# Performance work log

Measured on AMD Instinct MI355X. Metric: run time of the kernel, lower is better.

The kernel has to match this reference:

```python
import jax, jax.numpy as jnp
import numpy as np

B_NW, N, DIM, NH, DH, HID, NW, WH = 2048, 64, 512, 16, 32, 384, 64, 8
EPS = 1e-12  # F.normalize eps

def _rel_coords_log(wh, ww):
    # torch.cartesian_prod order: i (rows) outer, j (cols) inner
    ii, jj = np.meshgrid(np.arange(wh), np.arange(ww), indexing='ij')
    coords = np.stack([ii.ravel(), jj.ravel()], axis=-1).astype(np.float32)  # [N,2]
    rel = coords[:, None, :] - coords[None, :, :]                            # [N,N,2]
    return (np.sign(rel) * np.log1p(np.abs(rel))).astype(np.float32)

def setup_inputs() -> dict:
    key = jax.random.key(0)
    ks = jax.random.split(key, 9)
    s = 0.02
    inner = NH * DH
    return {
        'x': jax.random.normal(ks[0], (B_NW, N, DIM), jnp.float32),
        'mask': jax.random.normal(ks[1], (NW, N, N), jnp.float32),
        'w_qkv': jax.random.normal(ks[2], (DIM, 3 * inner), jnp.float32) * s,
        'tau': jnp.ones((1, NH, 1, 1), jnp.float32),
        'mlp_w1': jax.random.normal(ks[3], (2, HID), jnp.float32) * s,
        'mlp_b1': jnp.zeros((HID,), jnp.float32),
        'mlp_w2': jax.random.normal(ks[4], (HID, NH), jnp.float32) * s,
        'mlp_b2': jnp.zeros((NH,), jnp.float32),
        'w_out': jax.random.normal(ks[5], (inner, DIM), jnp.float32) * s,
        'b_out': jnp.zeros((DIM,), jnp.float32),
        'rel_log': jnp.asarray(_rel_coords_log(WH, WH)),
    }

def reference(x, mask, w_qkv, tau, mlp_w1, mlp_b1, mlp_w2, mlp_b2, w_out, b_out, rel_log):
    b, n, _ = x.shape
    qkv = x @ w_qkv                                   # [b, n, 3*nh*dh]
    qkv = qkv.reshape(b, n, 3, NH, DH)
    q, k, v = (jnp.transpose(qkv[:, :, i], (0, 2, 1, 3)) for i in range(3))  # [b, nh, n, dh]
    # cosine attention: L2-normalize q and k along head dim
    q = q / jnp.maximum(jnp.linalg.norm(q, axis=-1, keepdims=True), EPS)
    k = k / jnp.maximum(jnp.linalg.norm(k, axis=-1, keepdims=True), EPS)
    sim = jnp.einsum('bhid,bhjd->bhij', q, k) * tau   # learned temperature
    # relative position bias via meta MLP: [N,N,2] -> [N,N,nh]
    bias = jax.nn.relu(rel_log @ mlp_w1 + mlp_b1) @ mlp_w2 + mlp_b2
    sim = sim + jnp.transpose(bias, (2, 0, 1))[None]  # [1, nh, N, N]
    nw = mask.shape[0]
    sim = sim.reshape(b // nw, nw, NH, n, n) + mask[None, :, None]
    sim = sim.reshape(b, NH, n, n)
    attn = jax.nn.softmax(sim, axis=-1)
    out = jnp.einsum('bhij,bhjd->bhid', attn, v)
    out = jnp.transpose(out, (0, 2, 1, 3)).reshape(b, n, NH * DH)
    return out @ w_out + b_out
```

## Files before the change

### kernel.cpp

```cpp
#include <hip/hip_runtime.h>
#include <hip/hip_bf16.h>


typedef __bf16 bf16;
typedef __bf16 v4bf __attribute__((ext_vector_type(4)));
typedef __bf16 v8bf __attribute__((ext_vector_type(8)));
typedef float  v4f  __attribute__((ext_vector_type(4)));

__global__ void convert_x_kernel(const float* __restrict__ x, bf16* __restrict__ xbf) {
    const int stride = gridDim.x * 256;
    for (size_t idx = blockIdx.x * 256 + threadIdx.x; idx < 8388608; idx += stride) {
        const float4* xv = (const float4*)x;
        float4 v0 = xv[idx * 2];
        float4 v1 = xv[idx * 2 + 1];
        v8bf o = { (bf16)v0.x, (bf16)v0.y, (bf16)v0.z, (bf16)v0.w,
                   (bf16)v1.x, (bf16)v1.y, (bf16)v1.z, (bf16)v1.w };
        *(v8bf*)(xbf + idx * 8) = o;
    }
}

__global__ void convert_w_kernel(const float* __restrict__ wqkv, const float* __restrict__ wout,
                                 bf16* __restrict__ Wt, bf16* __restrict__ WoT) {
    int idx = blockIdx.x * 256 + threadIdx.x;
    Wt[idx] = (bf16)wqkv[(idx & 511) * 1536 + (idx >> 9)];
    if (idx < 262144) WoT[idx] = (bf16)wout[(idx & 511) * 512 + (idx >> 9)];
}

__global__ void bias_kernel(const float* __restrict__ rel_log, const float* __restrict__ w1,
                            const float* __restrict__ b1, const float* __restrict__ w2,
                            const float* __restrict__ b2, float* __restrict__ bias) {
    int p = blockIdx.x * 256 + threadIdx.x;
    float ra = rel_log[p * 2 + 0];
    float rb = rel_log[p * 2 + 1];
    float acc[16];
    #pragma unroll
    for (int t = 0; t < 16; ++t) acc[t] = 0.f;
    for (int kk = 0; kk < 384; ++kk) {
        float hv = fmaxf(ra * w1[kk] + rb * w1[384 + kk] + b1[kk], 0.f);
        #pragma unroll
        for (int t = 0; t < 16; ++t) acc[t] += hv * w2[kk * 16 + t];
    }
    #pragma unroll
    for (int t = 0; t < 16; ++t) bias[t * 4096 + p] = acc[t] + b2[t];
}

__global__ void comb_kernel(const float* __restrict__ bias, const float* __restrict__ mask,
                            float* __restrict__ comb) {
    int idx = blockIdx.x * 256 + threadIdx.x;
    int t = idx & 4095, wh = idx >> 12;
    int w = wh >> 4, h = wh & 15;
    int ij = t >> 8, rem = t & 255;
    int q16 = rem >> 2, r = t & 3;
    int lq = q16 >> 4, lm = q16 & 15;
    int i = ij >> 2, j = ij & 3;
    int p = (i * 16 + lq * 4 + r) * 64 + j * 16 + lm;
    comb[idx] = bias[h * 4096 + p] + mask[w * 4096 + p];
}

__global__ __launch_bounds__(256) void qkv_gemm_kernel(
    const bf16* __restrict__ xbf,
    const bf16* __restrict__ Wt,
    const float* __restrict__ tau,
    bf16* __restrict__ q_ws, bf16* __restrict__ k_ws, bf16* __restrict__ v_ws)
{
    __shared__ alignas(16) bf16 Alds[2][128 * 32];
    __shared__ alignas(16) bf16 Blds[2][128 * 32];
    const int bid = blockIdx.x, nwg = gridDim.x;
    const int wid = (bid & 7) * (nwg >> 3) + (bid >> 3);
    const int nb = wid % 12, mb = wid / 12;

    const int t = threadIdx.x;
    const int wv = t >> 6, lane = t & 63, lq = lane >> 4, lm = lane & 15;
    const int wr = wv >> 1, wc = wv & 1;

    const char* aBase = (const char*)xbf + (size_t)mb * 128 * 1024;
    const char* bBase = (const char*)Wt + (size_t)nb * 128 * 1024;

    auto stage = [&](int buf, int kt) {
        #pragma unroll
        for (int p = 0; p < 2; ++p) {
            int idx = (p * 4 + wv) * 1024 + lane * 16;
            int row = idx >> 6, kb = idx & 63;
            __builtin_amdgcn_global_load_lds(
                (const __attribute__((address_space(1))) void*)(aBase + (size_t)row * 1024 + kt * 64 + kb),
                (__attribute__((address_space(3))) void*)((char*)Alds + buf * 8192 + (p * 4 + wv) * 1024),
                16, 0, 0);
            __builtin_amdgcn_global_load_lds(
                (const __attribute__((address_space(1))) void*)(bBase + (size_t)row * 1024 + kt * 64 + kb),
                (__attribute__((address_space(3))) void*)((char*)Blds + buf * 8192 + (p * 4 + wv) * 1024),
                16, 0, 0);
        }
    };

    v4f acc[4][4];
    #pragma unroll
    for (int i = 0; i < 4; ++i)
        #pragma unroll
        for (int j = 0; j < 4; ++j) acc[i][j] = v4f{0.f, 0.f, 0.f, 0.f};

    stage(0, 0);
    __syncthreads();
    int cur = 0;
    for (int kt = 0; kt < 16; ++kt) {
        if (kt < 15) stage(cur ^ 1, kt + 1);
        v8bf af[4], bfj[4];
        #pragma unroll
        for (int i = 0; i < 4; ++i)
            af[i] = *(const v8bf*)(&Alds[cur][0] + (wr * 64 + i * 16 + lm) * 32 + lq * 8);
        #pragma unroll
        for (int j = 0; j < 4; ++j)
            bfj[j] = *(const v8bf*)(&Blds[cur][0] + (wc * 64 + j * 16 + lm) * 32 + lq * 8);
        #pragma unroll
        for (int i = 0; i < 4; ++i)
            #pragma unroll
            for (int j = 0; j < 4; ++j)
                acc[i][j] = __builtin_amdgcn_mfma_f32_16x16x32_bf16(af[i], bfj[j], acc[i][j], 0, 0, 0);
        __syncthreads();
        cur ^= 1;
    }

    const int bw = mb * 2 + wr;
    if (nb < 8) {
        bf16* dst = (nb < 4) ? q_ws : k_ws;
        const int hbase = (nb & 3) * 4 + wc * 2;
        #pragma unroll
        for (int tpair = 0; tpair < 2; ++tpair) {
            const int h = hbase + tpair;
            const float sc_top = (nb < 4) ? tau[h] : 1.0f;
            #pragma unroll
            for (int i = 0; i < 4; ++i)
                #pragma unroll
                for (int r = 0; r < 4; ++r) {
                    float a0 = acc[i][2 * tpair][r], a1 = acc[i][2 * tpair + 1][r];
                    float ss = a0 * a0 + a1 * a1;
                    #pragma unroll
                    for (int m = 1; m < 16; m <<= 1) ss += __shfl_xor(ss, m);
                    float sc = sc_top / fmaxf(sqrtf(ss), 1e-12f);
                    int n = i * 16 + lq * 4 + r;
                    size_t base = ((size_t)(bw * 16 + h) * 64 + n) * 32;
                    dst[base + lm]      = (bf16)(a0 * sc);
                    dst[base + 16 + lm] = (bf16)(a1 * sc);
                }
        }
    } else {
        #pragma unroll
        for (int j = 0; j < 4; ++j) {
            const int h = (nb - 8) * 4 + wc * 2 + (j >> 1);
            const int dh = (j & 1) * 16 + lm;
            #pragma unroll
            for (int i = 0; i < 4; ++i) {
                v4bf pv = { (bf16)acc[i][j][0], (bf16)acc[i][j][1],
                            (bf16)acc[i][j][2], (bf16)acc[i][j][3] };
                *(v4bf*)(v_ws + ((size_t)(bw * 16 + h) * 32 + dh) * 64 + i * 16 + lq * 4) = pv;
            }
        }
    }
}

__global__ __launch_bounds__(256) void attn_kernel(
    const bf16* __restrict__ q_ws,
    const bf16* __restrict__ k_ws,
    const bf16* __restrict__ v_ws,
    const float* __restrict__ comb,
    int wofs,
    bf16* __restrict__ attn_out)
{
    __shared__ alignas(16) bf16 P_all[4][64 * 72];
    const int blk = blockIdx.x;
    const int b = blk >> 2, g = blk & 3;
    const int tid = threadIdx.x;
    const int wv = tid >> 6, lane = tid & 63, lq = lane >> 4, lm = lane & 15;
    const int h = g * 4 + wv;
    const v4f z4 = {0.f, 0.f, 0.f, 0.f};

    bf16* P = P_all[wv];
    const size_t qk_base = (size_t)(b * 16 + h) * 64 * 32;
    const float* comb_hw = comb + ((size_t)(((wofs + b) & 63) * 16 + h)) * 4096
                                + (lq * 16 + lm) * 4;

    v8bf qf[4], kf[4];
    #pragma unroll
    for (int i = 0; i < 4; ++i)
        qf[i] = *(const v8bf*)(q_ws + qk_base + (i * 16 + lm) * 32 + lq * 8);
    #pragma unroll
    for (int j = 0; j < 4; ++j)
        kf[j] = *(const v8bf*)(k_ws + qk_base + (j * 16 + lm) * 32 + lq * 8);

    v4f s[4][4];
    #pragma unroll
    for (int i = 0; i < 4; ++i)
        #pragma unroll
        for (int j = 0; j < 4; ++j)
            s[i][j] = __builtin_amdgcn_mfma_f32_16x16x32_bf16(qf[i], kf[j], z4, 0, 0, 0);

    #pragma unroll
    for (int i = 0; i < 4; ++i)
        #pragma unroll
        for (int j = 0; j < 4; ++j) {
            float4 cv = *(const float4*)(comb_hw + (i * 4 + j) * 256);
            s[i][j][0] += cv.x; s[i][j][1] += cv.y;
            s[i][j][2] += cv.z; s[i][j][3] += cv.w;
        }

    float rcpl[4][4];
    #pragma unroll
    for (int i = 0; i < 4; ++i) {
        float mx[4], sm[4];
        #pragma unroll
        for (int r = 0; r < 4; ++r) {
            mx[r] = fmaxf(fmaxf(s[i][0][r], s[i][1][r]), fmaxf(s[i][2][r], s[i][3][r]));
            #pragma unroll
            for (int m = 1; m < 16; m <<= 1) mx[r] = fmaxf(mx[r], __shfl_xor(mx[r], m));
            sm[r] = 0.f;
        }
        #pragma unroll
        for (int j = 0; j < 4; ++j)
            #pragma unroll
            for (int r = 0; r < 4; ++r) {
                s[i][j][r] = __expf(s[i][j][r] - mx[r]);
                sm[r] += s[i][j][r];
            }
        #pragma unroll
        for (int r = 0; r < 4; ++r) {
            #pragma unroll
            for (int m = 1; m < 16; m <<= 1) sm[r] += __shfl_xor(sm[r], m);
            rcpl[i][r] = 1.0f / sm[r];
        }
    }

    #pragma unroll
    for (int i = 0; i < 4; ++i)
        #pragma unroll
        for (int j = 0; j < 4; ++j)
            #pragma unroll
            for (int r = 0; r < 4; ++r)
                P[(i * 16 + lq * 4 + r) * 72 + j * 16 + lm] = (bf16)s[i][j][r];

    const size_t v_base = (size_t)(b * 16 + h) * 32 * 64;
    v4f o[4][2];
    #pragma unroll
    for (int i = 0; i < 4; ++i)
        #pragma unroll
        for (int nt = 0; nt < 2; ++nt) o[i][nt] = z4;
    #pragma unroll
    for (int kk = 0; kk < 2; ++kk) {
        v8bf vf[2], pf[4];
        #pragma unroll
        for (int nt = 0; nt < 2; ++nt)
            vf[nt] = *(const v8bf*)(v_ws + v_base + (nt * 16 + lm) * 64 + kk * 32 + lq * 8);
        #pragma unroll
        for (int i = 0; i < 4; ++i)
            pf[i] = *(const v8bf*)(P + (i * 16 + lm) * 72 + kk * 32 + lq * 8);
        #pragma unroll
        for (int i = 0; i < 4; ++i)
            #pragma unroll
            for (int nt = 0; nt < 2; ++nt)
                o[i][nt] = __builtin_amdgcn_mfma_f32_16x16x32_bf16(pf[i], vf[nt], o[i][nt], 0, 0, 0);
    }
    #pragma unroll
    for (int i = 0; i < 4; ++i)
        #pragma unroll
        for (int nt = 0; nt < 2; ++nt)
            #pragma unroll
            for (int r = 0; r < 4; ++r)
                attn_out[(size_t)(b * 64 + i * 16 + lq * 4 + r) * 512 + h * 32 + nt * 16 + lm] =
                    (bf16)(o[i][nt][r] * rcpl[i][r]);
}

__global__ __launch_bounds__(256) void proj_gemm_kernel(
    const bf16* __restrict__ A,
    const bf16* __restrict__ Bt,
    const float* __restrict__ b_out,
    float* __restrict__ out)
{
    __shared__ alignas(16) bf16 Alds[2][128 * 32];
    __shared__ alignas(16) bf16 Blds[2][128 * 32];
    const int bid = blockIdx.x;
    const int wid = (bid & 7) * 512 + (bid >> 3);
    const int mb = wid >> 2, nb = wid & 3;
    const int tid = threadIdx.x;
    const int wv = tid >> 6, lane = tid & 63, lq = lane >> 4, lm = lane & 15;
    const int wr = wv >> 1, wc = wv & 1;

    const char* aBase = (const char*)A + (size_t)mb * 128 * 1024;
    const char* bBase = (const char*)Bt + (size_t)nb * 128 * 1024;

    auto stage = [&](int buf, int kt) {
        #pragma unroll
        for (int p = 0; p < 2; ++p) {
            int idx = (p * 4 + wv) * 1024 + lane * 16;
            int row = idx >> 6, kb = idx & 63;
            __builtin_amdgcn_global_load_lds(
                (const __attribute__((address_space(1))) void*)(aBase + (size_t)row * 1024 + kt * 64 + kb),
                (__attribute__((address_space(3))) void*)((char*)Alds + buf * 8192 + (p * 4 + wv) * 1024),
                16, 0, 0);
            __builtin_amdgcn_global_load_lds(
                (const __attribute__((address_space(1))) void*)(bBase + (size_t)row * 1024 + kt * 64 + kb),
                (__attribute__((address_space(3))) void*)((char*)Blds + buf * 8192 + (p * 4 + wv) * 1024),
                16, 0, 0);
        }
    };

    v4f acc[4][4];
    #pragma unroll
    for (int i = 0; i < 4; ++i)
        #pragma unroll
        for (int j = 0; j < 4; ++j) acc[i][j] = v4f{0.f, 0.f, 0.f, 0.f};

    stage(0, 0);
    __syncthreads();
    int cur = 0;
    for (int kt = 0; kt < 16; ++kt) {
        if (kt < 15) stage(cur ^ 1, kt + 1);
        v8bf af[4], bfj[4];
        #pragma unroll
        for (int i = 0; i < 4; ++i)
            af[i] = *(const v8bf*)(&Alds[cur][0] + (wr * 64 + i * 16 + lm) * 32 + lq * 8);
        #pragma unroll
        for (int j = 0; j < 4; ++j)
            bfj[j] = *(const v8bf*)(&Blds[cur][0] + (wc * 64 + j * 16 + lm) * 32 + lq * 8);
        #pragma unroll
        for (int i = 0; i < 4; ++i)
            #pragma unroll
            for (int j = 0; j < 4; ++j)
                acc[i][j] = __builtin_amdgcn_mfma_f32_16x16x32_bf16(af[i], bfj[j], acc[i][j], 0, 0, 0);
        __syncthreads();
        cur ^= 1;
    }

    #pragma unroll
    for (int j = 0; j < 4; ++j) {
        int col = nb * 128 + wc * 64 + j * 16 + lm;
        float bo = b_out[col];
        #pragma unroll
        for (int i = 0; i < 4; ++i)
            #pragma unroll
            for (int r = 0; r < 4; ++r)
                out[(size_t)(mb * 128 + wr * 64 + i * 16 + lq * 4 + r) * 512 + col] = acc[i][j][r] + bo;
    }
}

extern "C" void kernel_launch(void* const* d_in, const int* in_sizes, int n_in,
                              void* d_out, int out_size, void* d_ws, size_t ws_size,
                              hipStream_t stream) {
    (void)in_sizes; (void)n_in; (void)out_size;
    const float* x       = (const float*)d_in[0];
    const float* mask    = (const float*)d_in[1];
    const float* w_qkv   = (const float*)d_in[2];
    const float* tau     = (const float*)d_in[3];
    const float* mlp_w1  = (const float*)d_in[4];
    const float* mlp_b1  = (const float*)d_in[5];
    const float* mlp_w2  = (const float*)d_in[6];
    const float* mlp_b2  = (const float*)d_in[7];
    const float* w_out   = (const float*)d_in[8];
    const float* b_out   = (const float*)d_in[9];
    const float* rel_log = (const float*)d_in[10];
    float* out = (float*)d_out;

    char* ws = (char*)d_ws;
    bf16*  Wt     = (bf16*)(ws);
    bf16*  WoT    = (bf16*)(ws + 1572864);
    float* bias   = (float*)(ws + 2097152);
    float* comb   = (float*)(ws + 2359296);
    bf16*  shared = (bf16*)(ws + 19136512);
    char*  qkv_base = ws + 153354240;

    size_t avail = (ws_size > 153354240ULL) ? ws_size - 153354240ULL : 0;
    int W = 1024;
    while (W > 128 && (size_t)W * 196608ULL > avail) W >>= 1;
    const size_t qkbuf = (size_t)W * 65536;
    bf16* qb = (bf16*)qkv_base;
    bf16* kb = (bf16*)(qkv_base + qkbuf);
    bf16* vb = (bf16*)(qkv_base + 2 * qkbuf);

    convert_w_kernel<<<3072, 256, 0, stream>>>(w_qkv, w_out, Wt, WoT);
    bias_kernel<<<16, 256, 0, stream>>>(rel_log, mlp_w1, mlp_b1, mlp_w2, mlp_b2, bias);
    comb_kernel<<<16384, 256, 0, stream>>>(bias, mask, comb);
    convert_x_kernel<<<2048, 256, 0, stream>>>(x, shared);

    const int nchunk = 2048 / W;
    for (int c = 0; c < nchunk; ++c) {
        bf16* slice = shared + (size_t)c * W * 64 * 512;
        qkv_gemm_kernel<<<6 * W, 256, 0, stream>>>(slice, Wt, tau, qb, kb, vb);
        attn_kernel<<<4 * W, 256, 0, stream>>>(qb, kb, vb, comb, c * W, slice);
    }
    proj_gemm_kernel<<<4096, 256, 0, stream>>>(shared, WoT, b_out, out);
}
```

Measured before the change: 849.7 us.

## Move q/k normalization into attention and compute transposed scores for cheaper softmax

Removes the per-row L2 normalization (16-lane shuffle reductions) from the QKV GEMM epilogue and instead normalizes q and k fragments in the attention kernel, where each row needs only two cross-lane shuffles. The score matrix is now computed as K·Qᵀ so each lane holds a query row's values along the register axis, which makes the softmax max and sum reductions mostly in-register with two shuffles. The combined bias/mask layout is permuted to match. P is written to shared memory with vectorized 4-wide stores, already normalized, so the final output scaling goes away. Normalization now happens after bf16 rounding of raw q/k, which slightly changes precision, and the bias permutation must exactly match the new fragment layout.

```diff
diff --git a/kernel.cpp b/kernel.cpp
--- a/kernel.cpp
+++ b/kernel.cpp
@@ -49,18 +49,17 @@
     int idx = blockIdx.x * 256 + threadIdx.x;
     int t = idx & 4095, wh = idx >> 12;
     int w = wh >> 4, h = wh & 15;
-    int ij = t >> 8, rem = t & 255;
+    int ji = t >> 8, rem = t & 255;
+    int j = ji >> 2, i = ji & 3;
     int q16 = rem >> 2, r = t & 3;
     int lq = q16 >> 4, lm = q16 & 15;
-    int i = ij >> 2, j = ij & 3;
-    int p = (i * 16 + lq * 4 + r) * 64 + j * 16 + lm;
+    int p = (i * 16 + lm) * 64 + j * 16 + lq * 4 + r;
     comb[idx] = bias[h * 4096 + p] + mask[w * 4096 + p];
 }
 
 __global__ __launch_bounds__(256) void qkv_gemm_kernel(
     const bf16* __restrict__ xbf,
     const bf16* __restrict__ Wt,
-    const float* __restrict__ tau,
     bf16* __restrict__ q_ws, bf16* __restrict__ k_ws, bf16* __restrict__ v_ws)
 {
     __shared__ alignas(16) bf16 Alds[2][128 * 32];
@@ -126,20 +125,14 @@
         #pragma unroll
         for (int tpair = 0; tpair < 2; ++tpair) {
             const int h = hbase + tpair;
-            const float sc_top = (nb < 4) ? tau[h] : 1.0f;
             #pragma unroll
             for (int i = 0; i < 4; ++i)
                 #pragma unroll
                 for (int r = 0; r < 4; ++r) {
-                    float a0 = acc[i][2 * tpair][r], a1 = acc[i][2 * tpair + 1][r];
-                    float ss = a0 * a0 + a1 * a1;
-                    #pragma unroll
-                    for (int m = 1; m < 16; m <<= 1) ss += __shfl_xor(ss, m);
-                    float sc = sc_top / fmaxf(sqrtf(ss), 1e-12f);
                     int n = i * 16 + lq * 4 + r;
                     size_t base = ((size_t)(bw * 16 + h) * 64 + n) * 32;
-                    dst[base + lm]      = (bf16)(a0 * sc);
-                    dst[base + 16 + lm] = (bf16)(a1 * sc);
+                    dst[base + lm]      = (bf16)acc[i][2 * tpair][r];
+                    dst[base + 16 + lm] = (bf16)acc[i][2 * tpair + 1][r];
                 }
         }
     } else {
@@ -162,6 +155,7 @@
     const bf16* __restrict__ k_ws,
     const bf16* __restrict__ v_ws,
     const float* __restrict__ comb,
+    const float* __restrict__ tau,
     int wofs,
     bf16* __restrict__ attn_out)
 {
@@ -177,6 +171,7 @@
     const size_t qk_base = (size_t)(b * 16 + h) * 64 * 32;
     const float* comb_hw = comb + ((size_t)(((wofs + b) & 63) * 16 + h)) * 4096
                                 + (lq * 16 + lm) * 4;
+    const float tau_h = tau[h];
 
     v8bf qf[4], kf[4];
     #pragma unroll
@@ -186,55 +181,69 @@
     for (int j = 0; j < 4; ++j)
         kf[j] = *(const v8bf*)(k_ws + qk_base + (j * 16 + lm) * 32 + lq * 8);
 
-    v4f s[4][4];
-    #pragma unroll
-    for (int i = 0; i < 4; ++i)
+    #pragma unroll
+    for (int i = 0; i < 4; ++i) {
+        float a = 0.f;
+        #pragma unroll
+        for (int e = 0; e < 8; ++e) { float f = (float)qf[i][e]; a = fmaf(f, f, a); }
+        a += __shfl_xor(a, 16); a += __shfl_xor(a, 32);
+        float sc = tau_h / fmaxf(sqrtf(a), 1e-12f);
+        #pragma unroll
+        for (int e = 0; e < 8; ++e) qf[i][e] = (bf16)((float)qf[i][e] * sc);
+    }
+    #pragma unroll
+    for (int j = 0; j < 4; ++j) {
+        float a = 0.f;
+        #pragma unroll
+        for (int e = 0; e < 8; ++e) { float f = (float)kf[j][e]; a = fmaf(f, f, a); }
+        a += __shfl_xor(a, 16); a += __shfl_xor(a, 32);
+        float sc = 1.0f / fmaxf(sqrtf(a), 1e-12f);
+        #pragma unroll
+        for (int e = 0; e < 8; ++e) kf[j][e] = (bf16)((float)kf[j][e] * sc);
+    }
+
+    v4f st[4][4];
+    #pragma unroll
+    for (int j = 0; j < 4; ++j)
+        #pragma unroll
+        for (int i = 0; i < 4; ++i)
+            st[j][i] = __builtin_amdgcn_mfma_f32_16x16x32_bf16(kf[j], qf[i], z4, 0, 0, 0);
+
+    #pragma unroll
+    for (int j = 0; j < 4; ++j)
+        #pragma unroll
+        for (int i = 0; i < 4; ++i) {
+            float4 cv = *(const float4*)(comb_hw + (j * 4 + i) * 256);
+            st[j][i][0] += cv.x; st[j][i][1] += cv.y;
+            st[j][i][2] += cv.z; st[j][i][3] += cv.w;
+        }
+
+    #pragma unroll
+    for (int i = 0; i < 4; ++i) {
+        float mx = st[0][i][0];
         #pragma unroll
         for (int j = 0; j < 4; ++j)
-            s[i][j] = __builtin_amdgcn_mfma_f32_16x16x32_bf16(qf[i], kf[j], z4, 0, 0, 0);
-
-    #pragma unroll
-    for (int i = 0; i < 4; ++i)
+            #pragma unroll
+            for (int r = 0; r < 4; ++r) mx = fmaxf(mx, st[j][i][r]);
+        mx = fmaxf(mx, __shfl_xor(mx, 16));
+        mx = fmaxf(mx, __shfl_xor(mx, 32));
+        float sm = 0.f;
+        #pragma unroll
+        for (int j = 0; j < 4; ++j)
+            #pragma unroll
+            for (int r = 0; r < 4; ++r) {
+                float e = __expf(st[j][i][r] - mx);
+                st[j][i][r] = e; sm += e;
+            }
+        sm += __shfl_xor(sm, 16); sm += __shfl_xor(sm, 32);
+        float rcp = 1.0f / sm;
         #pragma unroll
         for (int j = 0; j < 4; ++j) {
-            float4 cv = *(const float4*)(comb_hw + (i * 4 + j) * 256);
-            s[i][j][0] += cv.x; s[i][j][1] += cv.y;
-            s[i][j][2] += cv.z; s[i][j][3] += cv.w;
-        }
-
-    float rcpl[4][4];
-    #pragma unroll
-    for (int i = 0; i < 4; ++i) {
-        float mx[4], sm[4];
-        #pragma unroll
-        for (int r = 0; r < 4; ++r) {
-            mx[r] = fmaxf(fmaxf(s[i][0][r], s[i][1][r]), fmaxf(s[i][2][r], s[i][3][r]));
-            #pragma unroll
-            for (int m = 1; m < 16; m <<= 1) mx[r] = fmaxf(mx[r], __shfl_xor(mx[r], m));
-            sm[r] = 0.f;
-        }
-        #pragma unroll
-        for (int j = 0; j < 4; ++j)
-            #pragma unroll
-            for (int r = 0; r < 4; ++r) {
-                s[i][j][r] = __expf(s[i][j][r] - mx[r]);
-                sm[r] += s[i][j][r];
-            }
-        #pragma unroll
-        for (int r = 0; r < 4; ++r) {
-            #pragma unroll
-            for (int m = 1; m < 16; m <<= 1) sm[r] += __shfl_xor(sm[r], m);
-            rcpl[i][r] = 1.0f / sm[r];
-        }
-    }
-
-    #pragma unroll
-    for (int i = 0; i < 4; ++i)
-        #pragma unroll
-        for (int j = 0; j < 4; ++j)
-            #pragma unroll
-            for (int r = 0; r < 4; ++r)
-                P[(i * 16 + lq * 4 + r) * 72 + j * 16 + lm] = (bf16)s[i][j][r];
+            v4bf pv = { (bf16)(st[j][i][0] * rcp), (bf16)(st[j][i][1] * rcp),
+                        (bf16)(st[j][i][2] * rcp), (bf16)(st[j][i][3] * rcp) };
+            *(v4bf*)(P + (i * 16 + lm) * 72 + j * 16 + lq * 4) = pv;
+        }
+    }
 
     const size_t v_base = (size_t)(b * 16 + h) * 32 * 64;
     v4f o[4][2];
@@ -264,7 +273,7 @@
             #pragma unroll
             for (int r = 0; r < 4; ++r)
                 attn_out[(size_t)(b * 64 + i * 16 + lq * 4 + r) * 512 + h * 32 + nt * 16 + lm] =
-                    (bf16)(o[i][nt][r] * rcpl[i][r]);
+                    (bf16)o[i][nt][r];
 }
 
 __global__ __launch_bounds__(256) void proj_gemm_kernel(
@@ -381,8 +390,8 @@
     const int nchunk = 2048 / W;
     for (int c = 0; c < nchunk; ++c) {
         bf16* slice = shared + (size_t)c * W * 64 * 512;
-        qkv_gemm_kernel<<<6 * W, 256, 0, stream>>>(slice, Wt, tau, qb, kb, vb);
-        attn_kernel<<<4 * W, 256, 0, stream>>>(qb, kb, vb, comb, c * W, slice);
+        qkv_gemm_kernel<<<6 * W, 256, 0, stream>>>(slice, Wt, qb, kb, vb);
+        attn_kernel<<<4 * W, 256, 0, stream>>>(qb, kb, vb, comb, tau, c * W, slice);
     }
     proj_gemm_kernel<<<4096, 256, 0, stream>>>(shared, WoT, b_out, out);
 }
```

Measured after the change: 777.5 us. 1.09x faster.
